# Kernel optimization log

Hardware: AMD Instinct MI355X
Metric: run time of the kernel (lower is better)

Reference implementation:

```python
import jax, jax.numpy as jnp
import numpy as np

B = 512      # number of agents (batch)
H = 64       # hidden_size
E = 64       # embadding_size
HP = 64      # relative-position embedding size in social pooling
OBS = 8      # observed track length
PRE = 12     # predict_length (pre_frame)


def setup_inputs() -> dict:
    key = jax.random.key(0)
    ks = jax.random.split(key, 10)
    def rn(k, shape, s=0.1):
        return jax.random.normal(k, shape, dtype=jnp.float32) * s
    return {
        "hidden_state": rn(ks[0], (1, B, H), 1.0),   # social hidden state from encoder
        "group_track": rn(ks[1], (B, OBS, 2), 1.0),  # ragged tracks regularized to OBS steps
        "W_emb": rn(ks[2], (2, E)),  "b_emb": jnp.zeros((E,), jnp.float32),
        "W_ih": rn(ks[3], (3 * H, E)), "W_hh": rn(ks[4], (3 * H, H)),
        "b_ih": jnp.zeros((3 * H,), jnp.float32), "b_hh": jnp.zeros((3 * H,), jnp.float32),
        "W_pos": rn(ks[5], (H, 2)), "b_pos": jnp.zeros((2,), jnp.float32),
        "W_rel": rn(ks[6], (2, HP)), "b_rel": jnp.zeros((HP,), jnp.float32),
        "W_pool": rn(ks[7], (HP + H, H)), "b_pool": jnp.zeros((H,), jnp.float32),
    }


def _gru_step(x, h, W_ih, W_hh, b_ih, b_hh):
    # torch nn.GRU single-layer step. x:[B,E], h:[B,H]
    gi = x @ W_ih.T + b_ih  # [B,3H]
    gh = h @ W_hh.T + b_hh
    i_r, i_z, i_n = jnp.split(gi, 3, axis=-1)
    h_r, h_z, h_n = jnp.split(gh, 3, axis=-1)
    r = jax.nn.sigmoid(i_r + h_r)
    z = jax.nn.sigmoid(i_z + h_z)
    n = jnp.tanh(i_n + r * h_n)
    return (1.0 - z) * n + z * h


def _spool(h, last_pos, W_rel, b_rel, W_pool, b_pool):
    # SGAN-style social pooling: embed pairwise relative last positions,
    # concat with each neighbor's hidden state, MLP, max-pool over neighbors.
    # h:[B,H], last_pos:[B,2] -> pooled:[B,H]
    rel = last_pos[None, :, :] - last_pos[:, None, :]          # [B,B,2]
    e = jax.nn.relu(rel @ W_rel + b_rel)                       # [B,B,HP]
    hj = jnp.broadcast_to(h[None, :, :], (h.shape[0], h.shape[0], h.shape[1]))
    feat = jnp.concatenate([e, hj], axis=-1)                   # [B,B,HP+H]
    m = jax.nn.relu(feat @ W_pool + b_pool)                    # [B,B,H]
    return jnp.max(m, axis=1)                                  # [B,H]


def reference(hidden_state, group_track, W_emb, b_emb, W_ih, W_hh, b_ih, b_hh,
              W_pos, b_pos, W_rel, b_rel, W_pool, b_pool):
    # Step 0: pool on encoder hidden state, GRU starts from zero state
    last = group_track[:, -1, :]                               # [B,2]
    pooled = _spool(hidden_state[0], last, W_rel, b_rel, W_pool, b_pool)
    pos0 = pooled @ W_pos + b_pos                              # [B,2]
    emb0 = pos0 @ W_emb + b_emb                                # [B,E]
    h0 = jnp.zeros((B, H), dtype=hidden_state.dtype)
    h = _gru_step(emb0, h0, W_ih, W_hh, b_ih, b_hh)

    def step(carry, _):
        h, last = carry
        pooled = _spool(h, last, W_rel, b_rel, W_pool, b_pool)  # pooling_p_step == 1
        pos = pooled @ W_pos + b_pos                            # [B,2]
        emb = pos @ W_emb + b_emb
        h_new = _gru_step(emb, h, W_ih, W_hh, b_ih, b_hh)
        return (h_new, pos), pos

    (_, _), poses = jax.lax.scan(step, (h, pos0), None, length=PRE - 1)  # [PRE-1,B,2]
    all_pos = jnp.concatenate([pos0[None], poses], axis=0)               # [PRE,B,2]
    # group_track grows by one position per step -> [B, OBS+PRE, 2]
    return jnp.concatenate([group_track, jnp.transpose(all_pos, (1, 0, 2))], axis=1)
```

## Files before the change

### kernel.cpp

```cpp
#include <hip/hip_runtime.h>
#include <math.h>

#define NB   512
#define NH   64
#define OBS  8
#define PRE  12

#define OFF_WREL  0
#define OFF_BREL  128
#define OFF_BPOOL 192
#define OFF_WPOS  256
#define OFF_BPOS  384
#define OFF_WEMB  386
#define OFF_BEMB  514
#define OFF_BIH   578
#define OFF_BHH   770
#define OFF_FLAG  962
#define N_SMALL   963

typedef __bf16 bf16x8 __attribute__((ext_vector_type(8)));
typedef float  f32x4  __attribute__((ext_vector_type(4)));

union FragU { bf16x8 v; unsigned short u[8]; };

__device__ __forceinline__ float bf2f(unsigned short u) {
  unsigned int x = ((unsigned int)u) << 16;
  return __builtin_bit_cast(float, x);
}
__device__ __forceinline__ unsigned short f2bf(float f) {
  unsigned int u = __builtin_bit_cast(unsigned int, f);
  u += 0x7FFFu + ((u >> 16) & 1u);
  return (unsigned short)(u >> 16);
}
__device__ __forceinline__ float ldf(const void* p, int i, bool isf32) {
  return isf32 ? ((const float*)p)[i] : bf2f(((const unsigned short*)p)[i]);
}
__device__ __forceinline__ unsigned short ld16(const void* p, int i, bool isf32) {
  return isf32 ? f2bf(((const float*)p)[i]) : ((const unsigned short*)p)[i];
}
__device__ __forceinline__ void stout(void* p, int i, float v, bool isf32) {
  if (isf32) ((float*)p)[i] = v;
  else       ((unsigned short*)p)[i] = f2bf(v);
}

__global__ __launch_bounds__(64) void prep_kernel(
    const void* __restrict__ hidden_state,
    const void* __restrict__ group_track,
    const void* __restrict__ W_emb,  const void* __restrict__ b_emb,
    const void* __restrict__ W_ih,   const void* __restrict__ W_hh,
    const void* __restrict__ b_ih,   const void* __restrict__ b_hh,
    const void* __restrict__ W_pos,  const void* __restrict__ b_pos,
    const void* __restrict__ W_rel,  const void* __restrict__ b_rel,
    const void* __restrict__ W_pool, const void* __restrict__ b_pool,
    float* __restrict__ last0,
    unsigned short* __restrict__ hbf0,
    float* __restrict__ h_carry,
    float* __restrict__ WTf,
    unsigned short* __restrict__ Wp_bf,
    float* __restrict__ smallf,
    void* __restrict__ out)
{
  const int b = blockIdx.x;
  const int o = threadIdx.x;

  int bad = 0;
  const unsigned short* hs16 = (const unsigned short*)hidden_state;
  for (int k = o; k < 256; k += 64) {
    unsigned e = (hs16[k] >> 7) & 0xFFu;
    bad |= (e >= 0x8Eu) ? 1 : 0;
  }
  const bool isf32 = (__ballot(bad) != 0ULL);

  hbf0[b * 64 + o] = ld16(hidden_state, b * 64 + o, isf32);
  h_carry[b * 64 + o] = 0.0f;
  if (o < 16) stout(out, b * 40 + o, ldf(group_track, b * 16 + o, isf32), isf32);
  if (o < 2)  last0[b * 2 + o] = ldf(group_track, b * 16 + 14 + o, isf32);

  if (b < 384) {
    int u = b * 64 + o;
    int k = u / 384, c = u % 384;
    WTf[u] = (c < 192) ? ldf(W_ih, c * 64 + k, isf32)
                       : ldf(W_hh, (c - 192) * 64 + k, isf32);
  } else {
    int u = (b - 384) * 64 + o;
    Wp_bf[u] = ld16(W_pool, u, isf32);
  }

  if (b < 16) {
    int u = b * 64 + o;
    if (u < N_SMALL) {
      float v;
      if      (u < 128) v = ldf(W_rel,  u,        isf32);
      else if (u < 192) v = ldf(b_rel,  u - 128,  isf32);
      else if (u < 256) v = ldf(b_pool, u - 192,  isf32);
      else if (u < 384) v = ldf(W_pos,  u - 256,  isf32);
      else if (u < 386) v = ldf(b_pos,  u - 384,  isf32);
      else if (u < 514) v = ldf(W_emb,  u - 386,  isf32);
      else if (u < 578) v = ldf(b_emb,  u - 514,  isf32);
      else if (u < 770) v = ldf(b_ih,   u - 578,  isf32);
      else if (u < 962) v = ldf(b_hh,   u - 770,  isf32);
      else              v = isf32 ? 1.0f : 0.0f;
      smallf[u] = v;
    }
  }
}

__global__ __launch_bounds__(256) void pair_kernel(
    const float* __restrict__ smallf,
    const unsigned short* __restrict__ Wp_bf,
    const float* __restrict__ WTf,
    const float* __restrict__ last_in,
    float* __restrict__ last_out,
    const unsigned short* __restrict__ hbf_in,
    unsigned short* __restrict__ hbf_out,
    float* __restrict__ h_carry,
    void* __restrict__ out,
    int t)
{
  const int i    = blockIdx.x;
  const int tid  = threadIdx.x;
  const int lane = tid & 63;
  const int wave = tid >> 6;
  const int col  = lane & 15;
  const int quad = lane >> 4;

  __shared__ float red[4][64];

  const float2* lp = (const float2*)last_in;
  const float2  li = lp[i];

  float wr0[2][8], wr1[2][8], brl[2][8];
  #pragma unroll
  for (int ks = 0; ks < 2; ++ks) {
    int kb = ks * 32 + quad * 8;
    #pragma unroll
    for (int j = 0; j < 8; ++j) {
      wr0[ks][j] = smallf[OFF_WREL + kb + j];
      wr1[ks][j] = smallf[OFF_WREL + 64 + kb + j];
      brl[ks][j] = smallf[OFF_BREL + kb + j];
    }
  }
  float bp[4];
  #pragma unroll
  for (int nt = 0; nt < 4; ++nt) bp[nt] = smallf[OFF_BPOOL + nt * 16 + col];

  FragU bw[4][4];
  #pragma unroll
  for (int nt = 0; nt < 4; ++nt)
    #pragma unroll
    for (int ks = 0; ks < 4; ++ks)
      #pragma unroll
      for (int j = 0; j < 8; ++j)
        bw[nt][ks].u[j] = Wp_bf[(ks * 32 + quad * 8 + j) * 64 + nt * 16 + col];

  float vmax[4] = {0.f, 0.f, 0.f, 0.f};

  const int jb0 = wave * 128;
  for (int s = 0; s < 4; ++s) {
    const int jb = jb0 + s * 32;
    const int r0 = jb + col, r1 = r0 + 16;
    const float2 l0 = lp[r0], l1 = lp[r1];
    const float d0x = l0.x - li.x, d0y = l0.y - li.y;
    const float d1x = l1.x - li.x, d1y = l1.y - li.y;

    FragU aE[2][2];
    #pragma unroll
    for (int ks = 0; ks < 2; ++ks) {
      #pragma unroll
      for (int j = 0; j < 8; ++j) {
        float e0 = fmaxf(d0x * wr0[ks][j] + d0y * wr1[ks][j] + brl[ks][j], 0.f);
        float e1 = fmaxf(d1x * wr0[ks][j] + d1y * wr1[ks][j] + brl[ks][j], 0.f);
        aE[0][ks].u[j] = f2bf(e0);
        aE[1][ks].u[j] = f2bf(e1);
      }
    }
    bf16x8 aH[2][2];
    #pragma unroll
    for (int mt = 0; mt < 2; ++mt) {
      int jr = jb + mt * 16 + col;
      #pragma unroll
      for (int ks = 0; ks < 2; ++ks)
        aH[mt][ks] = *(const bf16x8*)(hbf_in + jr * 64 + ks * 32 + quad * 8);
    }

    f32x4 acc[2][4];
    #pragma unroll
    for (int mt = 0; mt < 2; ++mt)
      #pragma unroll
      for (int nt = 0; nt < 4; ++nt)
        acc[mt][nt] = (f32x4){0.f, 0.f, 0.f, 0.f};

    #pragma unroll
    for (int nt = 0; nt < 4; ++nt)
      #pragma unroll
      for (int mt = 0; mt < 2; ++mt) {
        acc[mt][nt] = __builtin_amdgcn_mfma_f32_16x16x32_bf16(aE[mt][0].v, bw[nt][0].v, acc[mt][nt], 0, 0, 0);
        acc[mt][nt] = __builtin_amdgcn_mfma_f32_16x16x32_bf16(aE[mt][1].v, bw[nt][1].v, acc[mt][nt], 0, 0, 0);
        acc[mt][nt] = __builtin_amdgcn_mfma_f32_16x16x32_bf16(aH[mt][0],   bw[nt][2].v, acc[mt][nt], 0, 0, 0);
        acc[mt][nt] = __builtin_amdgcn_mfma_f32_16x16x32_bf16(aH[mt][1],   bw[nt][3].v, acc[mt][nt], 0, 0, 0);
      }

    #pragma unroll
    for (int mt = 0; mt < 2; ++mt)
      #pragma unroll
      for (int nt = 0; nt < 4; ++nt)
        #pragma unroll
        for (int r = 0; r < 4; ++r) {
          float v = acc[mt][nt][r] + bp[nt];
          vmax[nt] = fmaxf(fmaxf(v, 0.f), vmax[nt]);
        }
  }

  #pragma unroll
  for (int nt = 0; nt < 4; ++nt) {
    vmax[nt] = fmaxf(vmax[nt], __shfl_xor(vmax[nt], 16, 64));
    vmax[nt] = fmaxf(vmax[nt], __shfl_xor(vmax[nt], 32, 64));
  }
  if (lane < 16) {
    #pragma unroll
    for (int nt = 0; nt < 4; ++nt) red[wave][nt * 16 + lane] = vmax[nt];
  }
  __syncthreads();

  if (tid < 64) {
    const int o = tid;
    const bool isf32 = (smallf[OFF_FLAG] != 0.0f);
    float pooled = fmaxf(fmaxf(red[0][o], red[1][o]), fmaxf(red[2][o], red[3][o]));
    float p0 = pooled * smallf[OFF_WPOS + o * 2 + 0];
    float p1 = pooled * smallf[OFF_WPOS + o * 2 + 1];
    #pragma unroll
    for (int sft = 32; sft >= 1; sft >>= 1) {
      p0 += __shfl_xor(p0, sft, 64);
      p1 += __shfl_xor(p1, sft, 64);
    }
    p0 += smallf[OFF_BPOS + 0];
    p1 += smallf[OFF_BPOS + 1];
    if (o == 0) {
      stout(out, i * 40 + (OBS + t) * 2 + 0, p0, isf32);
      stout(out, i * 40 + (OBS + t) * 2 + 1, p1, isf32);
      last_out[2 * i]     = p0;
      last_out[2 * i + 1] = p1;
    }
    float gir = 0.f, giz = 0.f, gin = 0.f, ghr = 0.f, ghz = 0.f, ghn = 0.f;
    #pragma unroll 8
    for (int k = 0; k < 64; ++k) {
      float ek = p0 * smallf[OFF_WEMB + k] + p1 * smallf[OFF_WEMB + 64 + k]
               + smallf[OFF_BEMB + k];
      float hk = h_carry[i * 64 + k];
      const float* w = WTf + k * 384;
      gir += ek * w[o];
      giz += ek * w[64 + o];
      gin += ek * w[128 + o];
      ghr += hk * w[192 + o];
      ghz += hk * w[256 + o];
      ghn += hk * w[320 + o];
    }
    gir += smallf[OFF_BIH + o];       ghr += smallf[OFF_BHH + o];
    giz += smallf[OFF_BIH + 64 + o];  ghz += smallf[OFF_BHH + 64 + o];
    gin += smallf[OFF_BIH + 128 + o]; ghn += smallf[OFF_BHH + 128 + o];
    float r = 1.f / (1.f + __expf(-(gir + ghr)));
    float z = 1.f / (1.f + __expf(-(giz + ghz)));
    float n = tanhf(gin + r * ghn);
    float hp = h_carry[i * 64 + o];
    float hn = (1.f - z) * n + z * hp;
    h_carry[i * 64 + o] = hn;
    hbf_out[i * 64 + o] = f2bf(hn);
  }
}

extern "C" void kernel_launch(void* const* d_in, const int* in_sizes, int n_in,
                              void* d_out, int out_size, void* d_ws, size_t ws_size,
                              hipStream_t stream) {
  (void)in_sizes; (void)n_in; (void)out_size; (void)ws_size;
  const void* hidden_state = d_in[0];
  const void* group_track  = d_in[1];
  const void* W_emb  = d_in[2];
  const void* b_emb  = d_in[3];
  const void* W_ih   = d_in[4];
  const void* W_hh   = d_in[5];
  const void* b_ih   = d_in[6];
  const void* b_hh   = d_in[7];
  const void* W_pos  = d_in[8];
  const void* b_pos  = d_in[9];
  const void* W_rel  = d_in[10];
  const void* b_rel  = d_in[11];
  const void* W_pool = d_in[12];
  const void* b_pool = d_in[13];

  char* ws = (char*)d_ws;
  float* last[2]          = {(float*)(ws + 0),      (float*)(ws + 4096)};
  unsigned short* hbf[2]  = {(unsigned short*)(ws + 8192),
                             (unsigned short*)(ws + 73728)};
  float* h_carry          = (float*)(ws + 139264);
  float* WTf              = (float*)(ws + 270336);
  unsigned short* Wp_bf   = (unsigned short*)(ws + 368640);
  float* smallf           = (float*)(ws + 385024);

  prep_kernel<<<512, 64, 0, stream>>>(hidden_state, group_track,
                                      W_emb, b_emb, W_ih, W_hh, b_ih, b_hh,
                                      W_pos, b_pos, W_rel, b_rel, W_pool, b_pool,
                                      last[0], hbf[0], h_carry, WTf, Wp_bf,
                                      smallf, d_out);
  for (int t = 0; t < PRE; ++t) {
    int p = t & 1;
    pair_kernel<<<512, 256, 0, stream>>>(smallf, Wp_bf, WTf,
                                         last[p], last[1 - p],
                                         hbf[p], hbf[1 - p],
                                         h_carry, d_out, t);
  }
}
```

Baseline: 266.1 us.

## Fuse prep and all timesteps into one cooperative persistent kernel with grid sync

Replaces the 13 separate launches (prep plus 12 per-step pair kernels) with a single cooperative kernel of 256 blocks × 512 threads. Each block handles two agents and uses grid.sync between the prep phase and between timesteps. The pooling weight fragments are loaded into registers once and reused across all steps, and neighbour positions are preloaded per step. The change removes per-launch overhead and repeated weight loads, at the cost of grid-wide barrier latency and a large per-thread register footprint under launch_bounds(512,2). If the cooperative launch fails, it falls back to the old multi-kernel path.

Result: slower. 552.9 us (+107.8%).

```diff
diff --git a/kernel.cpp b/kernel.cpp
--- a/kernel.cpp
+++ b/kernel.cpp
@@ -1,5 +1,8 @@
 #include <hip/hip_runtime.h>
+#include <hip/hip_cooperative_groups.h>
 #include <math.h>
+
+namespace cg = cooperative_groups;
 
 #define NB   512
 #define NH   64
@@ -43,26 +46,244 @@
   else       ((unsigned short*)p)[i] = f2bf(v);
 }
 
+struct FusedArgs {
+  const void *hidden_state, *group_track, *W_emb, *b_emb, *W_ih, *W_hh,
+             *b_ih, *b_hh, *W_pos, *b_pos, *W_rel, *b_rel, *W_pool, *b_pool;
+  float *last0, *last1;
+  unsigned short *hbf0, *hbf1;
+  float *h_carry, *WTf;
+  unsigned short *Wp_bf;
+  float *smallf;
+  void *out;
+};
+
+__global__ __launch_bounds__(512, 2) void fused_kernel(FusedArgs a)
+{
+  cg::grid_group grid = cg::this_grid();
+  const int tid  = threadIdx.x;
+  const int lane = tid & 63;
+  const int wave = tid >> 6;
+  const int col  = lane & 15;
+  const int quad = lane >> 4;
+  const int gid  = blockIdx.x * 512 + tid;
+
+  __shared__ float red[8][64];
+
+  int bad = 0;
+  const unsigned short* hs16 = (const unsigned short*)a.hidden_state;
+  for (int k = lane; k < 256; k += 64) {
+    unsigned e = (hs16[k] >> 7) & 0xFFu;
+    bad |= (e >= 0x8Eu) ? 1 : 0;
+  }
+  const bool isf32 = (__ballot(bad) != 0ULL);
+
+  if (gid < 32768) {
+    int i = gid >> 6, o = gid & 63;
+    a.h_carry[gid] = 0.0f;
+    a.hbf0[gid] = ld16(a.hidden_state, gid, isf32);
+    if (o < 16) stout(a.out, i * 40 + o, ldf(a.group_track, i * 16 + o, isf32), isf32);
+    if (o < 2)  a.last0[i * 2 + o] = ldf(a.group_track, i * 16 + 14 + o, isf32);
+  } else if (gid < 57344) {
+    int u = gid - 32768;
+    int k = u / 384, c = u % 384;
+    a.WTf[u] = (c < 192) ? ldf(a.W_ih, c * 64 + k, isf32)
+                         : ldf(a.W_hh, (c - 192) * 64 + k, isf32);
+  } else if (gid < 65536) {
+    int u = gid - 57344;
+    a.Wp_bf[u] = ld16(a.W_pool, u, isf32);
+  } else if (gid < 65536 + N_SMALL) {
+    int u = gid - 65536;
+    float v;
+    if      (u < 128) v = ldf(a.W_rel,  u,        isf32);
+    else if (u < 192) v = ldf(a.b_rel,  u - 128,  isf32);
+    else if (u < 256) v = ldf(a.b_pool, u - 192,  isf32);
+    else if (u < 384) v = ldf(a.W_pos,  u - 256,  isf32);
+    else if (u < 386) v = ldf(a.b_pos,  u - 384,  isf32);
+    else if (u < 514) v = ldf(a.W_emb,  u - 386,  isf32);
+    else if (u < 578) v = ldf(a.b_emb,  u - 514,  isf32);
+    else if (u < 770) v = ldf(a.b_ih,   u - 578,  isf32);
+    else if (u < 962) v = ldf(a.b_hh,   u - 770,  isf32);
+    else              v = isf32 ? 1.0f : 0.0f;
+    a.smallf[u] = v;
+  }
+
+  grid.sync();
+
+  float wr0[2][8], wr1[2][8], brl[2][8];
+  #pragma unroll
+  for (int ks = 0; ks < 2; ++ks) {
+    int kb = ks * 32 + quad * 8;
+    #pragma unroll
+    for (int j = 0; j < 8; ++j) {
+      wr0[ks][j] = a.smallf[OFF_WREL + kb + j];
+      wr1[ks][j] = a.smallf[OFF_WREL + 64 + kb + j];
+      brl[ks][j] = a.smallf[OFF_BREL + kb + j];
+    }
+  }
+  float bp[4];
+  #pragma unroll
+  for (int nt = 0; nt < 4; ++nt) bp[nt] = a.smallf[OFF_BPOOL + nt * 16 + col];
+
+  FragU bw[4][4];
+  #pragma unroll
+  for (int nt = 0; nt < 4; ++nt)
+    #pragma unroll
+    for (int ks = 0; ks < 4; ++ks)
+      #pragma unroll
+      for (int j = 0; j < 8; ++j)
+        bw[nt][ks].u[j] = a.Wp_bf[(ks * 32 + quad * 8 + j) * 64 + nt * 16 + col];
+
+  const int iw  = 2 * blockIdx.x + (wave >> 2);
+  const int jb0 = (wave & 3) * 128;
+
+  for (int t = 0; t < PRE; ++t) {
+    const int p = t & 1;
+    const float* last_in  = p ? a.last1 : a.last0;
+    float*       last_out = p ? a.last0 : a.last1;
+    const unsigned short* hbf_in  = p ? a.hbf1 : a.hbf0;
+    unsigned short*       hbf_out = p ? a.hbf0 : a.hbf1;
+
+    const float2* lp = (const float2*)last_in;
+    const float2  li = lp[iw];
+
+    float2 l0s[4], l1s[4];
+    #pragma unroll
+    for (int s = 0; s < 4; ++s) {
+      l0s[s] = lp[jb0 + s * 32 + col];
+      l1s[s] = lp[jb0 + s * 32 + 16 + col];
+    }
+
+    float vmax[4] = {0.f, 0.f, 0.f, 0.f};
+
+    for (int s = 0; s < 4; ++s) {
+      const int jb = jb0 + s * 32;
+      const float d0x = l0s[s].x - li.x, d0y = l0s[s].y - li.y;
+      const float d1x = l1s[s].x - li.x, d1y = l1s[s].y - li.y;
+
+      bf16x8 aE[2][2];
+      #pragma unroll
+      for (int ks = 0; ks < 2; ++ks) {
+        #pragma unroll
+        for (int j = 0; j < 8; ++j) {
+          float e0 = fmaxf(fmaf(d0y, wr1[ks][j], fmaf(d0x, wr0[ks][j], brl[ks][j])), 0.f);
+          float e1 = fmaxf(fmaf(d1y, wr1[ks][j], fmaf(d1x, wr0[ks][j], brl[ks][j])), 0.f);
+          aE[0][ks][j] = (__bf16)e0;
+          aE[1][ks][j] = (__bf16)e1;
+        }
+      }
+      bf16x8 aH[2][2];
+      #pragma unroll
+      for (int mt = 0; mt < 2; ++mt) {
+        int jr = jb + mt * 16 + col;
+        #pragma unroll
+        for (int ks = 0; ks < 2; ++ks)
+          aH[mt][ks] = *(const bf16x8*)(hbf_in + jr * 64 + ks * 32 + quad * 8);
+      }
+
+      f32x4 acc[2][4];
+      #pragma unroll
+      for (int mt = 0; mt < 2; ++mt)
+        #pragma unroll
+        for (int nt = 0; nt < 4; ++nt)
+          acc[mt][nt] = (f32x4){0.f, 0.f, 0.f, 0.f};
+
+      #pragma unroll
+      for (int nt = 0; nt < 4; ++nt)
+        #pragma unroll
+        for (int mt = 0; mt < 2; ++mt) {
+          acc[mt][nt] = __builtin_amdgcn_mfma_f32_16x16x32_bf16(aE[mt][0], bw[nt][0].v, acc[mt][nt], 0, 0, 0);
+          acc[mt][nt] = __builtin_amdgcn_mfma_f32_16x16x32_bf16(aE[mt][1], bw[nt][1].v, acc[mt][nt], 0, 0, 0);
+          acc[mt][nt] = __builtin_amdgcn_mfma_f32_16x16x32_bf16(aH[mt][0], bw[nt][2].v, acc[mt][nt], 0, 0, 0);
+          acc[mt][nt] = __builtin_amdgcn_mfma_f32_16x16x32_bf16(aH[mt][1], bw[nt][3].v, acc[mt][nt], 0, 0, 0);
+        }
+
+      #pragma unroll
+      for (int mt = 0; mt < 2; ++mt)
+        #pragma unroll
+        for (int nt = 0; nt < 4; ++nt)
+          #pragma unroll
+          for (int r = 0; r < 4; ++r) {
+            float v = acc[mt][nt][r] + bp[nt];
+            vmax[nt] = fmaxf(fmaxf(v, 0.f), vmax[nt]);
+          }
+    }
+
+    #pragma unroll
+    for (int nt = 0; nt < 4; ++nt) {
+      vmax[nt] = fmaxf(vmax[nt], __shfl_xor(vmax[nt], 16, 64));
+      vmax[nt] = fmaxf(vmax[nt], __shfl_xor(vmax[nt], 32, 64));
+    }
+    if (lane < 16) {
+      #pragma unroll
+      for (int nt = 0; nt < 4; ++nt) red[wave][nt * 16 + lane] = vmax[nt];
+    }
+    __syncthreads();
+
+    if ((wave & 3) == 0) {
+      const int o = lane;
+      const int i = iw;
+      float pooled = fmaxf(fmaxf(red[wave][o], red[wave + 1][o]),
+                           fmaxf(red[wave + 2][o], red[wave + 3][o]));
+      float p0 = pooled * a.smallf[OFF_WPOS + o * 2 + 0];
+      float p1 = pooled * a.smallf[OFF_WPOS + o * 2 + 1];
+      #pragma unroll
+      for (int sft = 32; sft >= 1; sft >>= 1) {
+        p0 += __shfl_xor(p0, sft, 64);
+        p1 += __shfl_xor(p1, sft, 64);
+      }
+      p0 += a.smallf[OFF_BPOS + 0];
+      p1 += a.smallf[OFF_BPOS + 1];
+      if (o == 0) {
+        stout(a.out, i * 40 + (OBS + t) * 2 + 0, p0, isf32);
+        stout(a.out, i * 40 + (OBS + t) * 2 + 1, p1, isf32);
+        last_out[2 * i]     = p0;
+        last_out[2 * i + 1] = p1;
+      }
+      float gir = 0.f, giz = 0.f, gin = 0.f, ghr = 0.f, ghz = 0.f, ghn = 0.f;
+      #pragma unroll 8
+      for (int k = 0; k < 64; ++k) {
+        float ek = p0 * a.smallf[OFF_WEMB + k] + p1 * a.smallf[OFF_WEMB + 64 + k]
+                 + a.smallf[OFF_BEMB + k];
+        float hk = a.h_carry[i * 64 + k];
+        const float* w = a.WTf + k * 384;
+        gir += ek * w[o];
+        giz += ek * w[64 + o];
+        gin += ek * w[128 + o];
+        ghr += hk * w[192 + o];
+        ghz += hk * w[256 + o];
+        ghn += hk * w[320 + o];
+      }
+      gir += a.smallf[OFF_BIH + o];       ghr += a.smallf[OFF_BHH + o];
+      giz += a.smallf[OFF_BIH + 64 + o];  ghz += a.smallf[OFF_BHH + 64 + o];
+      gin += a.smallf[OFF_BIH + 128 + o]; ghn += a.smallf[OFF_BHH + 128 + o];
+      float r = 1.f / (1.f + __expf(-(gir + ghr)));
+      float z = 1.f / (1.f + __expf(-(giz + ghz)));
+      float n = tanhf(gin + r * ghn);
+      float hp = a.h_carry[i * 64 + o];
+      float hn = (1.f - z) * n + z * hp;
+      a.h_carry[i * 64 + o] = hn;
+      hbf_out[i * 64 + o] = f2bf(hn);
+    }
+
+    if (t < PRE - 1) grid.sync();
+  }
+}
+
 __global__ __launch_bounds__(64) void prep_kernel(
-    const void* __restrict__ hidden_state,
-    const void* __restrict__ group_track,
+    const void* __restrict__ hidden_state, const void* __restrict__ group_track,
     const void* __restrict__ W_emb,  const void* __restrict__ b_emb,
     const void* __restrict__ W_ih,   const void* __restrict__ W_hh,
     const void* __restrict__ b_ih,   const void* __restrict__ b_hh,
     const void* __restrict__ W_pos,  const void* __restrict__ b_pos,
     const void* __restrict__ W_rel,  const void* __restrict__ b_rel,
     const void* __restrict__ W_pool, const void* __restrict__ b_pool,
-    float* __restrict__ last0,
-    unsigned short* __restrict__ hbf0,
-    float* __restrict__ h_carry,
-    float* __restrict__ WTf,
-    unsigned short* __restrict__ Wp_bf,
-    float* __restrict__ smallf,
+    float* __restrict__ last0, unsigned short* __restrict__ hbf0,
+    float* __restrict__ h_carry, float* __restrict__ WTf,
+    unsigned short* __restrict__ Wp_bf, float* __restrict__ smallf,
     void* __restrict__ out)
 {
   const int b = blockIdx.x;
   const int o = threadIdx.x;
-
   int bad = 0;
   const unsigned short* hs16 = (const unsigned short*)hidden_state;
   for (int k = o; k < 256; k += 64) {
@@ -85,7 +306,6 @@
     int u = (b - 384) * 64 + o;
     Wp_bf[u] = ld16(W_pool, u, isf32);
   }
-
   if (b < 16) {
     int u = b * 64 + o;
     if (u < N_SMALL) {
@@ -109,13 +329,9 @@
     const float* __restrict__ smallf,
     const unsigned short* __restrict__ Wp_bf,
     const float* __restrict__ WTf,
-    const float* __restrict__ last_in,
-    float* __restrict__ last_out,
-    const unsigned short* __restrict__ hbf_in,
-    unsigned short* __restrict__ hbf_out,
-    float* __restrict__ h_carry,
-    void* __restrict__ out,
-    int t)
+    const float* __restrict__ last_in, float* __restrict__ last_out,
+    const unsigned short* __restrict__ hbf_in, unsigned short* __restrict__ hbf_out,
+    float* __restrict__ h_carry, void* __restrict__ out, int t)
 {
   const int i    = blockIdx.x;
   const int tid  = threadIdx.x;
@@ -154,26 +370,23 @@
         bw[nt][ks].u[j] = Wp_bf[(ks * 32 + quad * 8 + j) * 64 + nt * 16 + col];
 
   float vmax[4] = {0.f, 0.f, 0.f, 0.f};
-
   const int jb0 = wave * 128;
   for (int s = 0; s < 4; ++s) {
     const int jb = jb0 + s * 32;
-    const int r0 = jb + col, r1 = r0 + 16;
-    const float2 l0 = lp[r0], l1 = lp[r1];
+    const float2 l0 = lp[jb + col], l1 = lp[jb + 16 + col];
     const float d0x = l0.x - li.x, d0y = l0.y - li.y;
     const float d1x = l1.x - li.x, d1y = l1.y - li.y;
 
-    FragU aE[2][2];
-    #pragma unroll
-    for (int ks = 0; ks < 2; ++ks) {
+    bf16x8 aE[2][2];
+    #pragma unroll
+    for (int ks = 0; ks < 2; ++ks)
       #pragma unroll
       for (int j = 0; j < 8; ++j) {
-        float e0 = fmaxf(d0x * wr0[ks][j] + d0y * wr1[ks][j] + brl[ks][j], 0.f);
-        float e1 = fmaxf(d1x * wr0[ks][j] + d1y * wr1[ks][j] + brl[ks][j], 0.f);
-        aE[0][ks].u[j] = f2bf(e0);
-        aE[1][ks].u[j] = f2bf(e1);
-      }
-    }
+        float e0 = fmaxf(fmaf(d0y, wr1[ks][j], fmaf(d0x, wr0[ks][j], brl[ks][j])), 0.f);
+        float e1 = fmaxf(fmaf(d1y, wr1[ks][j], fmaf(d1x, wr0[ks][j], brl[ks][j])), 0.f);
+        aE[0][ks][j] = (__bf16)e0;
+        aE[1][ks][j] = (__bf16)e1;
+      }
     bf16x8 aH[2][2];
     #pragma unroll
     for (int mt = 0; mt < 2; ++mt) {
@@ -194,10 +407,10 @@
     for (int nt = 0; nt < 4; ++nt)
       #pragma unroll
       for (int mt = 0; mt < 2; ++mt) {
-        acc[mt][nt] = __builtin_amdgcn_mfma_f32_16x16x32_bf16(aE[mt][0].v, bw[nt][0].v, acc[mt][nt], 0, 0, 0);
-        acc[mt][nt] = __builtin_amdgcn_mfma_f32_16x16x32_bf16(aE[mt][1].v, bw[nt][1].v, acc[mt][nt], 0, 0, 0);
-        acc[mt][nt] = __builtin_amdgcn_mfma_f32_16x16x32_bf16(aH[mt][0],   bw[nt][2].v, acc[mt][nt], 0, 0, 0);
-        acc[mt][nt] = __builtin_amdgcn_mfma_f32_16x16x32_bf16(aH[mt][1],   bw[nt][3].v, acc[mt][nt], 0, 0, 0);
+        acc[mt][nt] = __builtin_amdgcn_mfma_f32_16x16x32_bf16(aE[mt][0], bw[nt][0].v, acc[mt][nt], 0, 0, 0);
+        acc[mt][nt] = __builtin_amdgcn_mfma_f32_16x16x32_bf16(aE[mt][1], bw[nt][1].v, acc[mt][nt], 0, 0, 0);
+        acc[mt][nt] = __builtin_amdgcn_mfma_f32_16x16x32_bf16(aH[mt][0], bw[nt][2].v, acc[mt][nt], 0, 0, 0);
+        acc[mt][nt] = __builtin_amdgcn_mfma_f32_16x16x32_bf16(aH[mt][1], bw[nt][3].v, acc[mt][nt], 0, 0, 0);
       }
 
     #pragma unroll
@@ -296,16 +509,32 @@
   unsigned short* Wp_bf   = (unsigned short*)(ws + 368640);
   float* smallf           = (float*)(ws + 385024);
 
-  prep_kernel<<<512, 64, 0, stream>>>(hidden_state, group_track,
-                                      W_emb, b_emb, W_ih, W_hh, b_ih, b_hh,
-                                      W_pos, b_pos, W_rel, b_rel, W_pool, b_pool,
-                                      last[0], hbf[0], h_carry, WTf, Wp_bf,
-                                      smallf, d_out);
-  for (int t = 0; t < PRE; ++t) {
-    int p = t & 1;
-    pair_kernel<<<512, 256, 0, stream>>>(smallf, Wp_bf, WTf,
-                                         last[p], last[1 - p],
-                                         hbf[p], hbf[1 - p],
-                                         h_carry, d_out, t);
-  }
-}
+  FusedArgs fa;
+  fa.hidden_state = hidden_state; fa.group_track = group_track;
+  fa.W_emb = W_emb; fa.b_emb = b_emb; fa.W_ih = W_ih; fa.W_hh = W_hh;
+  fa.b_ih = b_ih; fa.b_hh = b_hh; fa.W_pos = W_pos; fa.b_pos = b_pos;
+  fa.W_rel = W_rel; fa.b_rel = b_rel; fa.W_pool = W_pool; fa.b_pool = b_pool;
+  fa.last0 = last[0]; fa.last1 = last[1];
+  fa.hbf0 = hbf[0]; fa.hbf1 = hbf[1];
+  fa.h_carry = h_carry; fa.WTf = WTf; fa.Wp_bf = Wp_bf; fa.smallf = smallf;
+  fa.out = d_out;
+
+  void* params[] = { &fa };
+  hipError_t err = hipLaunchCooperativeKernel((const void*)fused_kernel,
+                                              dim3(256), dim3(512),
+                                              params, 0, stream);
+  if (err != hipSuccess) {
+    prep_kernel<<<512, 64, 0, stream>>>(hidden_state, group_track,
+                                        W_emb, b_emb, W_ih, W_hh, b_ih, b_hh,
+                                        W_pos, b_pos, W_rel, b_rel, W_pool, b_pool,
+                                        last[0], hbf[0], h_carry, WTf, Wp_bf,
+                                        smallf, d_out);
+    for (int t = 0; t < PRE; ++t) {
+      int p = t & 1;
+      pair_kernel<<<512, 256, 0, stream>>>(smallf, Wp_bf, WTf,
+                                           last[p], last[1 - p],
+                                           hbf[p], hbf[1 - p],
+                                           h_carry, d_out, t);
+    }
+  }
+}
```
